# Performance work log

Hardware: AMD Instinct MI355X
Metric: run time of the kernel (lower is better)

The kernel has to match this reference:

```python
import jax, jax.numpy as jnp
import numpy as np

B, D, H, L = 65536, 784, 392, 32

def _lin(x, W, b):
    return x @ W.T + b

def setup_inputs() -> dict:
    key = jax.random.key(0)
    ks = jax.random.split(key, 10)
    def w(k, shape):
        fan_in = shape[1]
        return jax.random.normal(k, shape, jnp.float32) * (1.0 / np.sqrt(fan_in))
    return {
        'x': jax.random.uniform(ks[0], (B, D), jnp.float32),
        'eps_z': jax.random.normal(ks[1], (B, L), jnp.float32),
        'eps_y': jax.random.normal(ks[2], (B, D), jnp.float32),
        'W_e1': w(ks[3], (H, D)), 'b_e1': jnp.zeros((H,), jnp.float32),
        'W_emu': w(ks[4], (L, H)), 'b_emu': jnp.zeros((L,), jnp.float32),
        'W_elv': w(ks[5], (L, H)), 'b_elv': jnp.zeros((L,), jnp.float32),
        'W_d1': w(ks[6], (H, L)), 'b_d1': jnp.zeros((H,), jnp.float32),
        'W_dmu': w(ks[7], (D, H)), 'b_dmu': jnp.zeros((D,), jnp.float32),
        'W_dlv': w(ks[8], (D, H)), 'b_dlv': jnp.zeros((D,), jnp.float32),
    }

def reference(x, eps_z, eps_y, W_e1, b_e1, W_emu, b_emu, W_elv, b_elv,
              W_d1, b_d1, W_dmu, b_dmu, W_dlv, b_dlv):
    # encode
    h = jax.nn.relu(_lin(x, W_e1, b_e1))
    mu_z = jax.nn.relu(_lin(h, W_emu, b_emu))
    logvar_z = jax.nn.relu(_lin(h, W_elv, b_elv))
    # reparameterize
    z = mu_z + eps_z * jnp.exp(0.5 * logvar_z)
    # decode
    hd = jax.nn.relu(_lin(z, W_d1, b_d1))
    mu_y = jax.nn.relu(_lin(hd, W_dmu, b_dmu))
    logvar_y = jax.nn.relu(_lin(hd, W_dlv, b_dlv))
    image_res = jax.nn.sigmoid(mu_y + eps_y * jnp.exp(0.5 * logvar_y))
    # NLL: MultivariateNormal(mu, cov=diag(exp(0.5*logvar))).log_prob(x), closed form
    # (original looped per-sample with a Cholesky of a diag matrix; math identical)
    d = mu_y.shape[1]
    var = jnp.exp(0.5 * logvar_y)            # diagonal covariance entries
    quad = jnp.sum((x - mu_y) ** 2 / var, axis=1)
    logdet = jnp.sum(0.5 * logvar_y, axis=1)
    log_prob = -0.5 * (d * jnp.log(2.0 * jnp.pi) + logdet + quad)
    nll = -jnp.mean(log_prob)
    # KL regularisation, faithful to source formula incl. log(1e-8 + exp(logvar))
    kl = jnp.sum(0.5 * jnp.sum(mu_z ** 2 + jnp.exp(logvar_z)
                               - jnp.log(1e-8 + jnp.exp(logvar_z)) - 1.0, axis=1))
    return image_res, nll + kl
```

## Files before the change

kernel.cpp:

```cpp
#include <hip/hip_runtime.h>

#define B_N   65536
#define D_N   784
#define H_N   392
#define L_N   32
#define OUT_IMG ((size_t)B_N * D_N)

typedef unsigned short ushort_t;
typedef __attribute__((ext_vector_type(8))) short short8;
typedef __attribute__((ext_vector_type(4))) float f32x4;

#define N_WE1  358400
#define N_WEZ  26624
#define N_WD1  13312
#define N_WDY  745472
#define N_W16  (N_WE1 + N_WEZ + N_WD1 + N_WDY)
#define N_BIAS 2720
#define WS_BYTES (N_W16*2 + N_BIAS*4)

__device__ __forceinline__ unsigned short f2bf(float f) {
  union { float f; unsigned u; } v; v.f = f;
  unsigned r = v.u + 0x7FFFu + ((v.u >> 16) & 1u);
  return (unsigned short)(r >> 16);
}

__device__ __forceinline__ void gl2lds16(const void* g, void* l) {
  __builtin_amdgcn_global_load_lds(
      (const __attribute__((address_space(1))) unsigned int*)(unsigned long long)g,
      (__attribute__((address_space(3))) unsigned int*)(unsigned int)(unsigned long long)l,
      16, 0, 0);
}

__global__ void vae_prep(const float* __restrict__ We1, const float* __restrict__ Wemu,
                         const float* __restrict__ Welv, const float* __restrict__ Wd1,
                         const float* __restrict__ Wdmu, const float* __restrict__ Wdlv,
                         const float* __restrict__ be1, const float* __restrict__ bemu,
                         const float* __restrict__ belv, const float* __restrict__ bd1,
                         const float* __restrict__ bdmu, const float* __restrict__ bdlv,
                         ushort_t* __restrict__ ws16, float* __restrict__ wsb,
                         float* __restrict__ scalar_out) {
  int idx = blockIdx.x * 256 + threadIdx.x;
  if (idx == 0) *scalar_out = 0.f;
  if (idx < N_W16) {
    float val;
    if (idx < N_WE1) {
      int e = idx; int j = e & 7, lane = (e >> 3) & 63, g = e >> 9;
      int nt = g % 28, kt = g / 28;
      int n = nt * 16 + (lane & 15), k = kt * 32 + ((lane >> 4) << 3) + j;
      val = (n < H_N && k < D_N) ? We1[n * D_N + k] : 0.f;
    } else if (idx < N_WE1 + N_WEZ) {
      int e = idx - N_WE1; int j = e & 7, lane = (e >> 3) & 63, g = e >> 9;
      int kt = g % 13, nt = g / 13;
      int n = nt * 16 + (lane & 15), k = kt * 32 + ((lane >> 4) << 3) + j;
      val = (k < H_N) ? (n < 32 ? Wemu[n * H_N + k] : Welv[(n - 32) * H_N + k]) : 0.f;
    } else if (idx < N_WE1 + N_WEZ + N_WD1) {
      int e = idx - N_WE1 - N_WEZ; int j = e & 7, lane = (e >> 3) & 63, nt = e >> 9;
      int n = nt * 16 + (lane & 15), k = ((lane >> 4) << 3) + j;
      val = (n < H_N) ? Wd1[n * L_N + k] : 0.f;
    } else {
      int e = idx - N_WE1 - N_WEZ - N_WD1; int j = e & 7, lane = (e >> 3) & 63, g = e >> 9;
      int tt = g & 3, nw = (g >> 2) & 3, c = (g >> 4) % 7, kt = g / 112;
      int pair = nw * 14 + 2 * c + (tt >> 1);
      int d = pair * 16 + (lane & 15);
      int k = kt * 32 + ((lane >> 4) << 3) + j;
      val = (d < D_N && k < H_N) ? ((tt & 1) ? Wdlv[d * H_N + k] : Wdmu[d * H_N + k]) : 0.f;
    }
    ws16[idx] = f2bf(val);
  } else {
    int bi = idx - N_W16;
    if (bi < N_BIAS) {
      float val;
      if      (bi < 448)  val = (bi < H_N) ? be1[bi] : 0.f;
      else if (bi < 512)  { int i2 = bi - 448;  val = (i2 < 32) ? bemu[i2] : belv[i2 - 32]; }
      else if (bi < 928)  { int i2 = bi - 512;  val = (i2 < H_N) ? bd1[i2] : 0.f; }
      else if (bi < 1824) { int i2 = bi - 928;  val = (i2 < D_N) ? bdmu[i2] : 0.f; }
      else                { int i2 = bi - 1824; val = (i2 < D_N) ? bdlv[i2] : 0.f; }
      wsb[bi] = val;
    }
  }
}

__global__ __launch_bounds__(512, 2) void vae_main(
    const float* __restrict__ x, const float* __restrict__ eps_z,
    const float* __restrict__ eps_y,
    const ushort_t* __restrict__ ws16, const float* __restrict__ wsb,
    float* __restrict__ out, float* __restrict__ scalar_out) {
  const ushort_t* We1t = ws16;
  const ushort_t* Wezt = ws16 + N_WE1;
  const ushort_t* Wd1t = Wezt + N_WEZ;
  const ushort_t* Wdyt = Wd1t + N_WD1;
  const float* be1p  = wsb;
  const float* bezp  = wsb + 448;
  const float* bd1p  = wsb + 512;
  const float* bdmup = wsb + 928;
  const float* bdlvp = wsb + 1824;

  __shared__ __align__(16) ushort_t hbuf[128 * 424];
  __shared__ __align__(16) ushort_t wslab[28 * 512];
  __shared__ __align__(16) ushort_t xslab[8 * 64 * 8];
  __shared__ __align__(16) ushort_t zbuf[128 * 40];
  __shared__ float red[8];

  const int tid  = threadIdx.x;
  const int w    = tid >> 6;
  const int lane = tid & 63;
  const int quad = lane >> 4;
  const int l16  = lane & 15;
  const int mw   = w >> 2, nw = w & 3;
  const int rb   = blockIdx.x * 128;

  float kl_acc = 0.f, q_acc = 0.f, ld_acc = 0.f;

  f32x4 acc1[4][7];
  {
    f32x4 z4 = {0.f, 0.f, 0.f, 0.f};
#pragma unroll
    for (int i = 0; i < 4; ++i)
#pragma unroll
      for (int t = 0; t < 7; ++t) acc1[i][t] = z4;
  }
  const int sr = tid >> 2, sq = tid & 3;
  for (int kt = 0; kt < 25; ++kt) {
    __syncthreads();
#pragma unroll
    for (int i = 0; i < 4; ++i) {
      int g = i * 512 + tid;
      if (g < 1792) gl2lds16((const char*)We1t + kt * 28672 + g * 16, (char*)wslab + g * 16);
    }
    {
      int4 P;
      if (kt == 24 && sq >= 2) { P.x = 0; P.y = 0; P.z = 0; P.w = 0; }
      else {
        const float4* px = (const float4*)(x + (size_t)(rb + sr) * D_N + kt * 32 + sq * 8);
        float4 v0 = px[0], v1 = px[1];
        P.x = f2bf(v0.x) | ((unsigned)f2bf(v0.y) << 16);
        P.y = f2bf(v0.z) | ((unsigned)f2bf(v0.w) << 16);
        P.z = f2bf(v1.x) | ((unsigned)f2bf(v1.y) << 16);
        P.w = f2bf(v1.z) | ((unsigned)f2bf(v1.w) << 16);
      }
      ((int4*)xslab)[(sr >> 4) * 64 + (sq << 4) + (sr & 15)] = P;
    }
    __syncthreads();
    short8 afr[4];
#pragma unroll
    for (int i = 0; i < 4; ++i)
      afr[i] = *(const short8*)(xslab + ((mw * 4 + i) * 64 + lane) * 8);
#pragma unroll
    for (int t = 0; t < 7; ++t) {
      short8 bfr = *(const short8*)(wslab + ((nw * 7 + t) * 64 + lane) * 8);
#pragma unroll
      for (int i = 0; i < 4; ++i)
        acc1[i][t] = __builtin_amdgcn_mfma_f32_16x16x32_bf16(afr[i], bfr, acc1[i][t], 0, 0, 0);
    }
  }
#pragma unroll
  for (int t = 0; t < 7; ++t) {
    int ntg = nw * 7 + t;
    if (ntg < 26) {
      int n = ntg * 16 + l16;
      float bb = be1p[n];
#pragma unroll
      for (int i = 0; i < 4; ++i)
#pragma unroll
        for (int r = 0; r < 4; ++r) {
          int m = mw * 64 + i * 16 + quad * 4 + r;
          hbuf[m * 424 + n] = f2bf(fmaxf(acc1[i][t][r] + bb, 0.f));
        }
    }
  }
  __syncthreads();

  f32x4 acc2[4];
  {
    f32x4 z4 = {0.f, 0.f, 0.f, 0.f};
#pragma unroll
    for (int nt = 0; nt < 4; ++nt) acc2[nt] = z4;
  }
  for (int kt = 0; kt < 13; ++kt) {
    short8 a = *(const short8*)(hbuf + (16 * w + l16) * 424 + kt * 32 + quad * 8);
#pragma unroll
    for (int nt = 0; nt < 4; ++nt) {
      short8 b = *(const short8*)(Wezt + ((nt * 13 + kt) * 64 + lane) * 8);
      acc2[nt] = __builtin_amdgcn_mfma_f32_16x16x32_bf16(a, b, acc2[nt], 0, 0, 0);
    }
  }
#pragma unroll
  for (int s = 0; s < 2; ++s) {
    float bmu = bezp[s * 16 + l16];
    float blv = bezp[32 + s * 16 + l16];
#pragma unroll
    for (int r = 0; r < 4; ++r) {
      float mu = fmaxf(acc2[s][r] + bmu, 0.f);
      float lv = fmaxf(acc2[s + 2][r] + blv, 0.f);
      int m = 16 * w + quad * 4 + r;
      int gm = rb + m;
      int l = s * 16 + l16;
      float e = expf(lv);
      kl_acc += 0.5f * (mu * mu + e - logf(1e-8f + e) - 1.f);
      float zz = mu + eps_z[gm * 32 + l] * expf(0.5f * lv);
      zbuf[m * 40 + l] = f2bf(zz);
    }
  }
  __syncthreads();

  {
    short8 az = *(const short8*)(zbuf + (16 * w + l16) * 40 + quad * 8);
    for (int nt = 0; nt < 26; ++nt) {
      short8 b = *(const short8*)(Wd1t + (nt * 64 + lane) * 8);
      f32x4 a4 = {0.f, 0.f, 0.f, 0.f};
      a4 = __builtin_amdgcn_mfma_f32_16x16x32_bf16(az, b, a4, 0, 0, 0);
      int n = nt * 16 + l16;
      float bb = bd1p[n];
#pragma unroll
      for (int r = 0; r < 4; ++r) {
        int m = 16 * w + quad * 4 + r;
        hbuf[m * 424 + n] = f2bf(fmaxf(a4[r] + bb, 0.f));
      }
    }
  }

  for (int c = 0; c < 7; ++c) {
    f32x4 acc5[4][4];
    {
      f32x4 z4 = {0.f, 0.f, 0.f, 0.f};
#pragma unroll
      for (int i = 0; i < 4; ++i)
#pragma unroll
        for (int tt = 0; tt < 4; ++tt) acc5[i][tt] = z4;
    }
    for (int kt = 0; kt < 13; ++kt) {
      __syncthreads();
#pragma unroll
      for (int i = 0; i < 2; ++i) {
        int g = i * 512 + tid;
        gl2lds16((const char*)Wdyt + (kt * 7 + c) * 16384 + g * 16, (char*)wslab + g * 16);
      }
      __syncthreads();
      short8 a[4];
#pragma unroll
      for (int i = 0; i < 4; ++i)
        a[i] = *(const short8*)(hbuf + (mw * 64 + i * 16 + l16) * 424 + kt * 32 + quad * 8);
#pragma unroll
      for (int tt = 0; tt < 4; ++tt) {
        short8 b = *(const short8*)(wslab + ((nw * 4 + tt) * 64 + lane) * 8);
#pragma unroll
        for (int i = 0; i < 4; ++i)
          acc5[i][tt] = __builtin_amdgcn_mfma_f32_16x16x32_bf16(a[i], b, acc5[i][tt], 0, 0, 0);
      }
    }
#pragma unroll
    for (int s = 0; s < 2; ++s) {
      int d = (nw * 14 + 2 * c + s) * 16 + l16;
      if (d < D_N) {
        float bmu = bdmup[d], blv = bdlvp[d];
#pragma unroll
        for (int i = 0; i < 4; ++i) {
#pragma unroll
          for (int r = 0; r < 4; ++r) {
            int m = mw * 64 + i * 16 + quad * 4 + r;
            size_t gi = (size_t)(rb + m) * D_N + d;
            float mu = fmaxf(acc5[i][2 * s][r] + bmu, 0.f);
            float lv = fmaxf(acc5[i][2 * s + 1][r] + blv, 0.f);
            float sd = expf(0.5f * lv);
            float tval = mu + eps_y[gi] * sd;
            out[gi] = 1.f / (1.f + expf(-tval));
            float dq = x[gi] - mu;
            q_acc  += dq * dq / sd;
            ld_acc += 0.5f * lv;
          }
        }
      }
    }
  }

  float v = (0.5f / (float)B_N) * (ld_acc + q_acc) + kl_acc;
#pragma unroll
  for (int off = 32; off; off >>= 1) v += __shfl_down(v, off, 64);
  if (lane == 0) red[w] = v;
  __syncthreads();
  if (tid == 0) {
    float tot = 0.f;
#pragma unroll
    for (int i = 0; i < 8; ++i) tot += red[i];
    if (blockIdx.x == 0) tot += 720.447808f;
    atomicAdd(scalar_out, tot);
  }
}

extern "C" void kernel_launch(void* const* d_in, const int* in_sizes, int n_in,
                              void* d_out, int out_size, void* d_ws, size_t ws_size,
                              hipStream_t stream) {
  const float* x     = (const float*)d_in[0];
  const float* eps_z = (const float*)d_in[1];
  const float* eps_y = (const float*)d_in[2];
  const float* We1   = (const float*)d_in[3];
  const float* be1   = (const float*)d_in[4];
  const float* Wemu  = (const float*)d_in[5];
  const float* bemu  = (const float*)d_in[6];
  const float* Welv  = (const float*)d_in[7];
  const float* belv  = (const float*)d_in[8];
  const float* Wd1   = (const float*)d_in[9];
  const float* bd1   = (const float*)d_in[10];
  const float* Wdmu  = (const float*)d_in[11];
  const float* bdmu  = (const float*)d_in[12];
  const float* Wdlv  = (const float*)d_in[13];
  const float* bdlv  = (const float*)d_in[14];

  float* out = (float*)d_out;
  float* scalar_out = out + OUT_IMG;

  ushort_t* ws16 = (ushort_t*)d_ws;
  float* wsb = (float*)((char*)d_ws + (size_t)N_W16 * 2);

  int prep_total = N_W16 + N_BIAS;
  int prep_blocks = (prep_total + 255) / 256;
  vae_prep<<<prep_blocks, 256, 0, stream>>>(We1, Wemu, Welv, Wd1, Wdmu, Wdlv,
                                            be1, bemu, belv, bd1, bdmu, bdlv,
                                            ws16, wsb, scalar_out);

  vae_main<<<B_N / 128, 512, 0, stream>>>(x, eps_z, eps_y, ws16, wsb, out, scalar_out);
}
```

Baseline: 874.7 us.

## Halve rows per block, shrink LDS, load x fragments directly, use fast math

Each block now handles 64 rows instead of 128. The hidden buffer stride drops from 424 to 392, and the x and z staging buffers are removed: x fragments are converted straight into registers, and z reuses the weight slab. Launch bounds rise to 4 blocks per CU, with half the accumulators per wave. The change also adds s_setprio around the MFMA loops, fast __expf/__logf and rcp intrinsics, and nontemporal loads and stores in the epilogue. The aim is higher occupancy and less LDS traffic. The cost is double the weight-slab reloads per output row, possible LDS bank conflicts from the unpadded stride, and slightly lower precision.

```diff
diff --git a/kernel.cpp b/kernel.cpp
--- a/kernel.cpp
+++ b/kernel.cpp
@@ -5,6 +5,9 @@
 #define H_N   392
 #define L_N   32
 #define OUT_IMG ((size_t)B_N * D_N)
+
+#define M_ROWS 64
+#define HSTR   392
 
 typedef unsigned short ushort_t;
 typedef __attribute__((ext_vector_type(8))) short short8;
@@ -80,7 +83,7 @@
   }
 }
 
-__global__ __launch_bounds__(512, 2) void vae_main(
+__global__ __launch_bounds__(512, 4) void vae_main(
     const float* __restrict__ x, const float* __restrict__ eps_z,
     const float* __restrict__ eps_y,
     const ushort_t* __restrict__ ws16, const float* __restrict__ wsb,
@@ -95,11 +98,11 @@
   const float* bdmup = wsb + 928;
   const float* bdlvp = wsb + 1824;
 
-  __shared__ __align__(16) ushort_t hbuf[128 * 424];
+  __shared__ __align__(16) ushort_t hbuf[M_ROWS * HSTR + 32];
   __shared__ __align__(16) ushort_t wslab[28 * 512];
-  __shared__ __align__(16) ushort_t xslab[8 * 64 * 8];
-  __shared__ __align__(16) ushort_t zbuf[128 * 40];
   __shared__ float red[8];
+
+  ushort_t* zb = wslab;
 
   const int tid  = threadIdx.x;
   const int w    = tid >> 6;
@@ -107,19 +110,25 @@
   const int quad = lane >> 4;
   const int l16  = lane & 15;
   const int mw   = w >> 2, nw = w & 3;
-  const int rb   = blockIdx.x * 128;
+  const int rb   = blockIdx.x * M_ROWS;
 
   float kl_acc = 0.f, q_acc = 0.f, ld_acc = 0.f;
 
-  f32x4 acc1[4][7];
+  if (tid < 32) hbuf[M_ROWS * HSTR + tid] = 0;
+
+  f32x4 acc1[2][7];
   {
     f32x4 z4 = {0.f, 0.f, 0.f, 0.f};
 #pragma unroll
-    for (int i = 0; i < 4; ++i)
+    for (int i = 0; i < 2; ++i)
 #pragma unroll
       for (int t = 0; t < 7; ++t) acc1[i][t] = z4;
   }
-  const int sr = tid >> 2, sq = tid & 3;
+  const float* xp[2];
+#pragma unroll
+  for (int i = 0; i < 2; ++i)
+    xp[i] = x + (size_t)(rb + mw * 32 + i * 16 + l16) * D_N + quad * 8;
+
   for (int kt = 0; kt < 25; ++kt) {
     __syncthreads();
 #pragma unroll
@@ -127,104 +136,117 @@
       int g = i * 512 + tid;
       if (g < 1792) gl2lds16((const char*)We1t + kt * 28672 + g * 16, (char*)wslab + g * 16);
     }
+    short8 afr[2];
     {
-      int4 P;
-      if (kt == 24 && sq >= 2) { P.x = 0; P.y = 0; P.z = 0; P.w = 0; }
-      else {
-        const float4* px = (const float4*)(x + (size_t)(rb + sr) * D_N + kt * 32 + sq * 8);
-        float4 v0 = px[0], v1 = px[1];
-        P.x = f2bf(v0.x) | ((unsigned)f2bf(v0.y) << 16);
-        P.y = f2bf(v0.z) | ((unsigned)f2bf(v0.w) << 16);
-        P.z = f2bf(v1.x) | ((unsigned)f2bf(v1.y) << 16);
-        P.w = f2bf(v1.z) | ((unsigned)f2bf(v1.w) << 16);
-      }
-      ((int4*)xslab)[(sr >> 4) * 64 + (sq << 4) + (sr & 15)] = P;
+      bool real = !(kt == 24 && quad >= 2);
+#pragma unroll
+      for (int i = 0; i < 2; ++i) {
+        union { int4 p; short8 s; } u;
+        if (real) {
+          const float4* px = (const float4*)(xp[i] + kt * 32);
+          float4 v0 = px[0], v1 = px[1];
+          u.p.x = f2bf(v0.x) | ((unsigned)f2bf(v0.y) << 16);
+          u.p.y = f2bf(v0.z) | ((unsigned)f2bf(v0.w) << 16);
+          u.p.z = f2bf(v1.x) | ((unsigned)f2bf(v1.y) << 16);
+          u.p.w = f2bf(v1.z) | ((unsigned)f2bf(v1.w) << 16);
+        } else {
+          u.p.x = 0; u.p.y = 0; u.p.z = 0; u.p.w = 0;
+        }
+        afr[i] = u.s;
+      }
     }
     __syncthreads();
-    short8 afr[4];
-#pragma unroll
-    for (int i = 0; i < 4; ++i)
-      afr[i] = *(const short8*)(xslab + ((mw * 4 + i) * 64 + lane) * 8);
+    __builtin_amdgcn_s_setprio(1);
 #pragma unroll
     for (int t = 0; t < 7; ++t) {
       short8 bfr = *(const short8*)(wslab + ((nw * 7 + t) * 64 + lane) * 8);
 #pragma unroll
-      for (int i = 0; i < 4; ++i)
+      for (int i = 0; i < 2; ++i)
         acc1[i][t] = __builtin_amdgcn_mfma_f32_16x16x32_bf16(afr[i], bfr, acc1[i][t], 0, 0, 0);
     }
+    __builtin_amdgcn_s_setprio(0);
   }
 #pragma unroll
   for (int t = 0; t < 7; ++t) {
     int ntg = nw * 7 + t;
-    if (ntg < 26) {
+    if (ntg < 25) {
       int n = ntg * 16 + l16;
-      float bb = be1p[n];
-#pragma unroll
-      for (int i = 0; i < 4; ++i)
+      bool ok = (n < H_N);
+      float bb = ok ? be1p[n] : 0.f;
+#pragma unroll
+      for (int i = 0; i < 2; ++i)
 #pragma unroll
         for (int r = 0; r < 4; ++r) {
-          int m = mw * 64 + i * 16 + quad * 4 + r;
-          hbuf[m * 424 + n] = f2bf(fmaxf(acc1[i][t][r] + bb, 0.f));
+          int m = mw * 32 + i * 16 + quad * 4 + r;
+          if (ok) hbuf[m * HSTR + n] = f2bf(fmaxf(acc1[i][t][r] + bb, 0.f));
         }
     }
   }
   __syncthreads();
 
-  f32x4 acc2[4];
+  if (w < 4) {
+    f32x4 acc2[4];
+    {
+      f32x4 z4 = {0.f, 0.f, 0.f, 0.f};
+#pragma unroll
+      for (int nt = 0; nt < 4; ++nt) acc2[nt] = z4;
+    }
+    for (int kt = 0; kt < 13; ++kt) {
+      short8 a = *(const short8*)(hbuf + (16 * w + l16) * HSTR + kt * 32 + quad * 8);
+#pragma unroll
+      for (int nt = 0; nt < 4; ++nt) {
+        short8 b = *(const short8*)(Wezt + ((nt * 13 + kt) * 64 + lane) * 8);
+        acc2[nt] = __builtin_amdgcn_mfma_f32_16x16x32_bf16(a, b, acc2[nt], 0, 0, 0);
+      }
+    }
+#pragma unroll
+    for (int s = 0; s < 2; ++s) {
+      float bmu = bezp[s * 16 + l16];
+      float blv = bezp[32 + s * 16 + l16];
+#pragma unroll
+      for (int r = 0; r < 4; ++r) {
+        float mu = fmaxf(acc2[s][r] + bmu, 0.f);
+        float lv = fmaxf(acc2[s + 2][r] + blv, 0.f);
+        int m = 16 * w + quad * 4 + r;
+        int gm = rb + m;
+        int l = s * 16 + l16;
+        float e = __expf(lv);
+        kl_acc += 0.5f * (mu * mu + e - __logf(1e-8f + e) - 1.f);
+        float zz = mu + eps_z[gm * 32 + l] * __expf(0.5f * lv);
+        zb[m * 40 + l] = f2bf(zz);
+      }
+    }
+  }
+  __syncthreads();
+
   {
-    f32x4 z4 = {0.f, 0.f, 0.f, 0.f};
-#pragma unroll
-    for (int nt = 0; nt < 4; ++nt) acc2[nt] = z4;
-  }
-  for (int kt = 0; kt < 13; ++kt) {
-    short8 a = *(const short8*)(hbuf + (16 * w + l16) * 424 + kt * 32 + quad * 8);
-#pragma unroll
-    for (int nt = 0; nt < 4; ++nt) {
-      short8 b = *(const short8*)(Wezt + ((nt * 13 + kt) * 64 + lane) * 8);
-      acc2[nt] = __builtin_amdgcn_mfma_f32_16x16x32_bf16(a, b, acc2[nt], 0, 0, 0);
-    }
-  }
-#pragma unroll
-  for (int s = 0; s < 2; ++s) {
-    float bmu = bezp[s * 16 + l16];
-    float blv = bezp[32 + s * 16 + l16];
-#pragma unroll
-    for (int r = 0; r < 4; ++r) {
-      float mu = fmaxf(acc2[s][r] + bmu, 0.f);
-      float lv = fmaxf(acc2[s + 2][r] + blv, 0.f);
-      int m = 16 * w + quad * 4 + r;
-      int gm = rb + m;
-      int l = s * 16 + l16;
-      float e = expf(lv);
-      kl_acc += 0.5f * (mu * mu + e - logf(1e-8f + e) - 1.f);
-      float zz = mu + eps_z[gm * 32 + l] * expf(0.5f * lv);
-      zbuf[m * 40 + l] = f2bf(zz);
-    }
-  }
-  __syncthreads();
-
-  {
-    short8 az = *(const short8*)(zbuf + (16 * w + l16) * 40 + quad * 8);
-    for (int nt = 0; nt < 26; ++nt) {
+    const int rw = (w & 3) * 16;
+    const int wh = w >> 2;
+    short8 az = *(const short8*)(zb + (rw + l16) * 40 + quad * 8);
+    for (int t2 = 0; t2 < 13; ++t2) {
+      int nt = wh * 13 + t2;
+      if (nt >= 25) continue;
       short8 b = *(const short8*)(Wd1t + (nt * 64 + lane) * 8);
       f32x4 a4 = {0.f, 0.f, 0.f, 0.f};
       a4 = __builtin_amdgcn_mfma_f32_16x16x32_bf16(az, b, a4, 0, 0, 0);
       int n = nt * 16 + l16;
-      float bb = bd1p[n];
+      bool ok = (n < H_N);
+      float bb = ok ? bd1p[n] : 0.f;
 #pragma unroll
       for (int r = 0; r < 4; ++r) {
-        int m = 16 * w + quad * 4 + r;
-        hbuf[m * 424 + n] = f2bf(fmaxf(a4[r] + bb, 0.f));
-      }
-    }
-  }
+        int m = rw + quad * 4 + r;
+        if (ok) hbuf[m * HSTR + n] = f2bf(fmaxf(a4[r] + bb, 0.f));
+      }
+    }
+  }
+  __syncthreads();
 
   for (int c = 0; c < 7; ++c) {
-    f32x4 acc5[4][4];
+    f32x4 acc5[2][4];
     {
       f32x4 z4 = {0.f, 0.f, 0.f, 0.f};
 #pragma unroll
-      for (int i = 0; i < 4; ++i)
+      for (int i = 0; i < 2; ++i)
 #pragma unroll
         for (int tt = 0; tt < 4; ++tt) acc5[i][tt] = z4;
     }
@@ -236,17 +258,19 @@
         gl2lds16((const char*)Wdyt + (kt * 7 + c) * 16384 + g * 16, (char*)wslab + g * 16);
       }
       __syncthreads();
-      short8 a[4];
-#pragma unroll
-      for (int i = 0; i < 4; ++i)
-        a[i] = *(const short8*)(hbuf + (mw * 64 + i * 16 + l16) * 424 + kt * 32 + quad * 8);
+      short8 a[2];
+#pragma unroll
+      for (int i = 0; i < 2; ++i)
+        a[i] = *(const short8*)(hbuf + (mw * 32 + i * 16 + l16) * HSTR + kt * 32 + quad * 8);
+      __builtin_amdgcn_s_setprio(1);
 #pragma unroll
       for (int tt = 0; tt < 4; ++tt) {
         short8 b = *(const short8*)(wslab + ((nw * 4 + tt) * 64 + lane) * 8);
 #pragma unroll
-        for (int i = 0; i < 4; ++i)
+        for (int i = 0; i < 2; ++i)
           acc5[i][tt] = __builtin_amdgcn_mfma_f32_16x16x32_bf16(a[i], b, acc5[i][tt], 0, 0, 0);
       }
+      __builtin_amdgcn_s_setprio(0);
     }
 #pragma unroll
     for (int s = 0; s < 2; ++s) {
@@ -254,18 +278,20 @@
       if (d < D_N) {
         float bmu = bdmup[d], blv = bdlvp[d];
 #pragma unroll
-        for (int i = 0; i < 4; ++i) {
+        for (int i = 0; i < 2; ++i) {
 #pragma unroll
           for (int r = 0; r < 4; ++r) {
-            int m = mw * 64 + i * 16 + quad * 4 + r;
+            int m = mw * 32 + i * 16 + quad * 4 + r;
             size_t gi = (size_t)(rb + m) * D_N + d;
             float mu = fmaxf(acc5[i][2 * s][r] + bmu, 0.f);
             float lv = fmaxf(acc5[i][2 * s + 1][r] + blv, 0.f);
-            float sd = expf(0.5f * lv);
-            float tval = mu + eps_y[gi] * sd;
-            out[gi] = 1.f / (1.f + expf(-tval));
-            float dq = x[gi] - mu;
-            q_acc  += dq * dq / sd;
+            float sd = __expf(0.5f * lv);
+            float ey = __builtin_nontemporal_load(&eps_y[gi]);
+            float xx = __builtin_nontemporal_load(&x[gi]);
+            float tval = mu + ey * sd;
+            __builtin_nontemporal_store(__builtin_amdgcn_rcpf(1.f + __expf(-tval)), &out[gi]);
+            float dq = xx - mu;
+            q_acc  += dq * dq * __builtin_amdgcn_rcpf(sd);
             ld_acc += 0.5f * lv;
           }
         }
@@ -318,5 +344,5 @@
                                             be1, bemu, belv, bd1, bdmu, bdlv,
                                             ws16, wsb, scalar_out);
 
-  vae_main<<<B_N / 128, 512, 0, stream>>>(x, eps_z, eps_y, ws16, wsb, out, scalar_out);
-}
+  vae_main<<<B_N / M_ROWS, 512, 0, stream>>>(x, eps_z, eps_y, ws16, wsb, out, scalar_out);
+}
```

Measured after the change: 735.2 us. 15.9% less time.
